# Performance work log

Measured on AMD Instinct MI355X. Metric: run time of the kernel, lower is better.

The kernel has to match this reference:

```python
import jax, jax.numpy as jnp
import numpy as np

D_IN = 1024
D_OUT = 1024
N = 4096


def setup_inputs() -> dict:
    key = jax.random.key(0)
    kx, kq, kk, kv = jax.random.split(key, 4)
    s = 1.0 / np.sqrt(D_IN)
    return {
        "x": jax.random.normal(kx, (N, D_IN), dtype=jnp.float32),
        # nn.Linear weights stored as [d_out, d_in]
        "wq": jax.random.uniform(kq, (D_OUT, D_IN), dtype=jnp.float32, minval=-s, maxval=s),
        "wk": jax.random.uniform(kk, (D_OUT, D_IN), dtype=jnp.float32, minval=-s, maxval=s),
        "wv": jax.random.uniform(kv, (D_OUT, D_IN), dtype=jnp.float32, minval=-s, maxval=s),
    }


def reference(x, wq, wk, wv):
    q = x @ wq.T  # [N, d_out]
    k = x @ wk.T
    v = x @ wv.T
    scores = q @ k.T  # [N, N]
    weights = jax.nn.softmax(scores / jnp.sqrt(jnp.asarray(k.shape[-1], x.dtype)), axis=-1)
    return weights @ v  # [N, d_out]
```

## Files before the change

kernel.cpp:

```cpp
#include <hip/hip_runtime.h>
#include <cstdint>

#define NTOK 4096
#define DMODEL 1024

typedef __bf16 bf16x8 __attribute__((ext_vector_type(8)));
typedef float f32x4 __attribute__((ext_vector_type(4)));

__device__ __forceinline__ unsigned short f32_to_bf16(float f) {
    unsigned int u = __float_as_uint(f);
    unsigned int r = 0x7FFFu + ((u >> 16) & 1u);
    return (unsigned short)((u + r) >> 16);
}

__global__ __launch_bounds__(256) void cvt_f32_bf16(const float* __restrict__ in,
                                                    unsigned short* __restrict__ out,
                                                    int n4) {
    int i = blockIdx.x * 256 + threadIdx.x;
    if (i >= n4) return;
    float4 v = reinterpret_cast<const float4*>(in)[i];
    ushort4 o;
    o.x = f32_to_bf16(v.x);
    o.y = f32_to_bf16(v.y);
    o.z = f32_to_bf16(v.z);
    o.w = f32_to_bf16(v.w);
    reinterpret_cast<ushort4*>(out)[i] = o;
}

#define BM 128
#define BN 128
#define BK 64

#define EPI_F32 0
#define EPI_BF16 1
#define EPI_BF16T 2

template <int EPI>
__global__ __launch_bounds__(256, 2) void gemm_nt(
    const unsigned short* __restrict__ A, const unsigned short* __restrict__ B,
    void* __restrict__ C, int K, int lda, int ldb, int ldc) {
    __shared__ __align__(16) unsigned short As[BM * BK];
    __shared__ __align__(16) unsigned short Bs[BN * BK];

    const int tid = threadIdx.x;
    const int lane = tid & 63;
    const int wave = tid >> 6;
    const int wr = wave >> 1, wc = wave & 1;

    const unsigned short* Ablk = A + (size_t)blockIdx.y * BM * lda;
    const unsigned short* Bblk = B + (size_t)blockIdx.x * BN * ldb;

    f32x4 acc[4][4] = {};

    for (int k0 = 0; k0 < K; k0 += BK) {
#pragma unroll
        for (int i = 0; i < 4; ++i) {
            const int c = tid + i * 256;
            const int row = c >> 3;
            const int jl = (c & 7) ^ (row & 7);
            const unsigned short* ga = Ablk + (size_t)row * lda + (k0 + jl * 8);
            const unsigned short* gb = Bblk + (size_t)row * ldb + (k0 + jl * 8);
            __builtin_amdgcn_global_load_lds(
                (const __attribute__((address_space(1))) void*)ga,
                (__attribute__((address_space(3))) void*)(&As[c * 8]), 16, 0, 0);
            __builtin_amdgcn_global_load_lds(
                (const __attribute__((address_space(1))) void*)gb,
                (__attribute__((address_space(3))) void*)(&Bs[c * 8]), 16, 0, 0);
        }
        __syncthreads();

#pragma unroll
        for (int ks = 0; ks < 2; ++ks) {
            bf16x8 af[4], bfr[4];
#pragma unroll
            for (int m = 0; m < 4; ++m) {
                const int row = wr * 64 + m * 16 + (lane & 15);
                const int ch = (ks * 4 + (lane >> 4)) ^ (row & 7);
                af[m] = *reinterpret_cast<const bf16x8*>(
                    reinterpret_cast<const char*>(As) + row * 128 + ch * 16);
            }
#pragma unroll
            for (int n = 0; n < 4; ++n) {
                const int row = wc * 64 + n * 16 + (lane & 15);
                const int ch = (ks * 4 + (lane >> 4)) ^ (row & 7);
                bfr[n] = *reinterpret_cast<const bf16x8*>(
                    reinterpret_cast<const char*>(Bs) + row * 128 + ch * 16);
            }
#pragma unroll
            for (int m = 0; m < 4; ++m)
#pragma unroll
                for (int n = 0; n < 4; ++n)
                    acc[m][n] = __builtin_amdgcn_mfma_f32_16x16x32_bf16(
                        af[m], bfr[n], acc[m][n], 0, 0, 0);
        }
        __syncthreads();
    }

    const int col0 = blockIdx.x * BN + wc * 64 + (lane & 15);
    const int row0 = blockIdx.y * BM + wr * 64 + ((lane >> 4) << 2);

    if (EPI == EPI_F32) {
        float* Cf = reinterpret_cast<float*>(C);
#pragma unroll
        for (int m = 0; m < 4; ++m)
#pragma unroll
            for (int n = 0; n < 4; ++n)
#pragma unroll
                for (int r = 0; r < 4; ++r)
                    Cf[(size_t)(row0 + m * 16 + r) * ldc + (col0 + n * 16)] = acc[m][n][r];
    } else if (EPI == EPI_BF16) {
        unsigned short* Cb = reinterpret_cast<unsigned short*>(C);
#pragma unroll
        for (int m = 0; m < 4; ++m)
#pragma unroll
            for (int n = 0; n < 4; ++n)
#pragma unroll
                for (int r = 0; r < 4; ++r)
                    Cb[(size_t)(row0 + m * 16 + r) * ldc + (col0 + n * 16)] =
                        f32_to_bf16(acc[m][n][r]);
    } else {
        unsigned short* Cb = reinterpret_cast<unsigned short*>(C);
#pragma unroll
        for (int m = 0; m < 4; ++m)
#pragma unroll
            for (int n = 0; n < 4; ++n) {
                ushort4 o;
                o.x = f32_to_bf16(acc[m][n][0]);
                o.y = f32_to_bf16(acc[m][n][1]);
                o.z = f32_to_bf16(acc[m][n][2]);
                o.w = f32_to_bf16(acc[m][n][3]);
                *reinterpret_cast<ushort4*>(
                    &Cb[(size_t)(col0 + n * 16) * ldc + (row0 + m * 16)]) = o;
            }
    }
}

__global__ __launch_bounds__(256) void softmax_rows(float* __restrict__ S, int N) {
    const int row = blockIdx.x;
    float* s = S + (size_t)row * N;
    const int t = threadIdx.x;

    float v[16];
    float mx = -1e30f;
#pragma unroll
    for (int i = 0; i < 4; ++i) {
        float4 x = reinterpret_cast<const float4*>(s)[t + i * 256];
        v[i * 4 + 0] = x.x;
        v[i * 4 + 1] = x.y;
        v[i * 4 + 2] = x.z;
        v[i * 4 + 3] = x.w;
        mx = fmaxf(mx, fmaxf(fmaxf(x.x, x.y), fmaxf(x.z, x.w)));
    }
#pragma unroll
    for (int off = 32; off; off >>= 1) mx = fmaxf(mx, __shfl_xor(mx, off));
    __shared__ float redm[4];
    if (!(t & 63)) redm[t >> 6] = mx;
    __syncthreads();
    mx = fmaxf(fmaxf(redm[0], redm[1]), fmaxf(redm[2], redm[3]));

    float sum = 0.f;
#pragma unroll
    for (int i = 0; i < 16; ++i) {
        v[i] = __expf((v[i] - mx) * 0.03125f);
        sum += v[i];
    }
#pragma unroll
    for (int off = 32; off; off >>= 1) sum += __shfl_xor(sum, off);
    __shared__ float reds[4];
    if (!(t & 63)) reds[t >> 6] = sum;
    __syncthreads();
    sum = (reds[0] + reds[1]) + (reds[2] + reds[3]);
    const float inv = 1.0f / sum;

    unsigned short* p = reinterpret_cast<unsigned short*>(s);
#pragma unroll
    for (int i = 0; i < 4; ++i) {
        ushort4 o;
        o.x = f32_to_bf16(v[i * 4 + 0] * inv);
        o.y = f32_to_bf16(v[i * 4 + 1] * inv);
        o.z = f32_to_bf16(v[i * 4 + 2] * inv);
        o.w = f32_to_bf16(v[i * 4 + 3] * inv);
        reinterpret_cast<ushort4*>(p)[t + i * 256] = o;
    }
}

extern "C" void kernel_launch(void* const* d_in, const int* in_sizes, int n_in,
                              void* d_out, int out_size, void* d_ws, size_t ws_size,
                              hipStream_t stream) {
    (void)in_sizes; (void)n_in; (void)out_size; (void)ws_size;
    const float* x = (const float*)d_in[0];
    const float* wq = (const float*)d_in[1];
    const float* wk = (const float*)d_in[2];
    const float* wv = (const float*)d_in[3];
    float* out = (float*)d_out;

    const size_t MB = 1ull << 20;
    char* w = (char*)d_ws;
    unsigned short* xb  = (unsigned short*)(w + 0 * MB);
    unsigned short* wqb = (unsigned short*)(w + 8 * MB);
    unsigned short* wkb = (unsigned short*)(w + 10 * MB);
    unsigned short* wvb = (unsigned short*)(w + 12 * MB);
    unsigned short* Qb  = (unsigned short*)(w + 14 * MB);
    unsigned short* Kb  = (unsigned short*)(w + 22 * MB);
    unsigned short* Vt  = (unsigned short*)(w + 30 * MB);
    float* S            = (float*)(w + 38 * MB);

    cvt_f32_bf16<<<4096, 256, 0, stream>>>(x, xb, (NTOK * DMODEL) / 4);
    cvt_f32_bf16<<<1024, 256, 0, stream>>>(wq, wqb, (DMODEL * DMODEL) / 4);
    cvt_f32_bf16<<<1024, 256, 0, stream>>>(wk, wkb, (DMODEL * DMODEL) / 4);
    cvt_f32_bf16<<<1024, 256, 0, stream>>>(wv, wvb, (DMODEL * DMODEL) / 4);

    dim3 gqkv(DMODEL / BN, NTOK / BM);
    gemm_nt<EPI_BF16><<<gqkv, 256, 0, stream>>>(xb, wqb, Qb, DMODEL, DMODEL, DMODEL, DMODEL);
    gemm_nt<EPI_BF16><<<gqkv, 256, 0, stream>>>(xb, wkb, Kb, DMODEL, DMODEL, DMODEL, DMODEL);
    gemm_nt<EPI_BF16T><<<gqkv, 256, 0, stream>>>(xb, wvb, Vt, DMODEL, DMODEL, DMODEL, NTOK);

    dim3 gs(NTOK / BN, NTOK / BM);
    gemm_nt<EPI_F32><<<gs, 256, 0, stream>>>(Qb, Kb, S, DMODEL, DMODEL, DMODEL, NTOK);

    softmax_rows<<<NTOK, 256, 0, stream>>>(S, NTOK);

    dim3 gpv(DMODEL / BN, NTOK / BM);
    gemm_nt<EPI_F32><<<gpv, 256, 0, stream>>>((const unsigned short*)S, Vt, out,
                                              NTOK, 2 * NTOK, NTOK, DMODEL);
}
```

Baseline: 264.0 us.

## Fuse QKV projections into one GEMM and split-K the PV GEMM with atomics

Concatenates the three bf16 weight matrices so Q, K and V come from a single 24x32-block GEMM launch, with Q and K interleaved in one [N,2048] buffer and V written transposed. The PV GEMM, which had only 256 blocks, is split four ways along K with fp32 atomic adds into an output that is zeroed first. This cuts launch count and raises parallelism on the small-grid GEMMs, at the cost of an extra memset, atomic traffic and a nondeterministic summation order.

```diff
diff --git a/kernel.cpp b/kernel.cpp
--- a/kernel.cpp
+++ b/kernel.cpp
@@ -31,17 +31,47 @@
 #define BN 128
 #define BK 64
 
-#define EPI_F32 0
-#define EPI_BF16 1
-#define EPI_BF16T 2
-
-template <int EPI>
-__global__ __launch_bounds__(256, 2) void gemm_nt(
+#define STAGE_TILES(Ablk, lda, Bblk, ldb, k0)                                        \
+    _Pragma("unroll") for (int i = 0; i < 4; ++i) {                                  \
+        const int c = tid + i * 256;                                                 \
+        const int row = c >> 3;                                                      \
+        const int jl = (c & 7) ^ (row & 7);                                          \
+        const unsigned short* ga = (Ablk) + (size_t)row * (lda) + ((k0) + jl * 8);   \
+        const unsigned short* gb = (Bblk) + (size_t)row * (ldb) + ((k0) + jl * 8);   \
+        __builtin_amdgcn_global_load_lds(                                            \
+            (const __attribute__((address_space(1))) void*)ga,                       \
+            (__attribute__((address_space(3))) void*)(&As[c * 8]), 16, 0, 0);        \
+        __builtin_amdgcn_global_load_lds(                                            \
+            (const __attribute__((address_space(1))) void*)gb,                       \
+            (__attribute__((address_space(3))) void*)(&Bs[c * 8]), 16, 0, 0);        \
+    }
+
+#define COMPUTE_TILE()                                                               \
+    _Pragma("unroll") for (int ks = 0; ks < 2; ++ks) {                               \
+        bf16x8 af[4], bfr[4];                                                        \
+        _Pragma("unroll") for (int m = 0; m < 4; ++m) {                              \
+            const int row = wr * 64 + m * 16 + (lane & 15);                          \
+            const int ch = (ks * 4 + (lane >> 4)) ^ (row & 7);                       \
+            af[m] = *reinterpret_cast<const bf16x8*>(                                \
+                reinterpret_cast<const char*>(As) + row * 128 + ch * 16);            \
+        }                                                                            \
+        _Pragma("unroll") for (int n = 0; n < 4; ++n) {                              \
+            const int row = wc * 64 + n * 16 + (lane & 15);                          \
+            const int ch = (ks * 4 + (lane >> 4)) ^ (row & 7);                       \
+            bfr[n] = *reinterpret_cast<const bf16x8*>(                               \
+                reinterpret_cast<const char*>(Bs) + row * 128 + ch * 16);            \
+        }                                                                            \
+        _Pragma("unroll") for (int m = 0; m < 4; ++m)                                \
+            _Pragma("unroll") for (int n = 0; n < 4; ++n)                            \
+                acc[m][n] = __builtin_amdgcn_mfma_f32_16x16x32_bf16(                 \
+                    af[m], bfr[n], acc[m][n], 0, 0, 0);                              \
+    }
+
+__global__ __launch_bounds__(256, 2) void gemm_nt_f32(
     const unsigned short* __restrict__ A, const unsigned short* __restrict__ B,
-    void* __restrict__ C, int K, int lda, int ldb, int ldc) {
+    float* __restrict__ C, int K, int lda, int ldb, int ldc) {
     __shared__ __align__(16) unsigned short As[BM * BK];
     __shared__ __align__(16) unsigned short Bs[BN * BK];
-
     const int tid = threadIdx.x;
     const int lane = tid & 63;
     const int wave = tid >> 6;
@@ -49,77 +79,62 @@
 
     const unsigned short* Ablk = A + (size_t)blockIdx.y * BM * lda;
     const unsigned short* Bblk = B + (size_t)blockIdx.x * BN * ldb;
-
     f32x4 acc[4][4] = {};
 
     for (int k0 = 0; k0 < K; k0 += BK) {
-#pragma unroll
-        for (int i = 0; i < 4; ++i) {
-            const int c = tid + i * 256;
-            const int row = c >> 3;
-            const int jl = (c & 7) ^ (row & 7);
-            const unsigned short* ga = Ablk + (size_t)row * lda + (k0 + jl * 8);
-            const unsigned short* gb = Bblk + (size_t)row * ldb + (k0 + jl * 8);
-            __builtin_amdgcn_global_load_lds(
-                (const __attribute__((address_space(1))) void*)ga,
-                (__attribute__((address_space(3))) void*)(&As[c * 8]), 16, 0, 0);
-            __builtin_amdgcn_global_load_lds(
-                (const __attribute__((address_space(1))) void*)gb,
-                (__attribute__((address_space(3))) void*)(&Bs[c * 8]), 16, 0, 0);
-        }
-        __syncthreads();
-
-#pragma unroll
-        for (int ks = 0; ks < 2; ++ks) {
-            bf16x8 af[4], bfr[4];
-#pragma unroll
-            for (int m = 0; m < 4; ++m) {
-                const int row = wr * 64 + m * 16 + (lane & 15);
-                const int ch = (ks * 4 + (lane >> 4)) ^ (row & 7);
-                af[m] = *reinterpret_cast<const bf16x8*>(
-                    reinterpret_cast<const char*>(As) + row * 128 + ch * 16);
-            }
-#pragma unroll
-            for (int n = 0; n < 4; ++n) {
-                const int row = wc * 64 + n * 16 + (lane & 15);
-                const int ch = (ks * 4 + (lane >> 4)) ^ (row & 7);
-                bfr[n] = *reinterpret_cast<const bf16x8*>(
-                    reinterpret_cast<const char*>(Bs) + row * 128 + ch * 16);
-            }
-#pragma unroll
-            for (int m = 0; m < 4; ++m)
-#pragma unroll
-                for (int n = 0; n < 4; ++n)
-                    acc[m][n] = __builtin_amdgcn_mfma_f32_16x16x32_bf16(
-                        af[m], bfr[n], acc[m][n], 0, 0, 0);
-        }
+        STAGE_TILES(Ablk, lda, Bblk, ldb, k0)
+        __syncthreads();
+        COMPUTE_TILE()
         __syncthreads();
     }
 
     const int col0 = blockIdx.x * BN + wc * 64 + (lane & 15);
     const int row0 = blockIdx.y * BM + wr * 64 + ((lane >> 4) << 2);
-
-    if (EPI == EPI_F32) {
-        float* Cf = reinterpret_cast<float*>(C);
+#pragma unroll
+    for (int m = 0; m < 4; ++m)
+#pragma unroll
+        for (int n = 0; n < 4; ++n)
+#pragma unroll
+            for (int r = 0; r < 4; ++r)
+                C[(size_t)(row0 + m * 16 + r) * ldc + (col0 + n * 16)] = acc[m][n][r];
+}
+
+__global__ __launch_bounds__(256, 2) void gemm_qkv(
+    const unsigned short* __restrict__ xb, const unsigned short* __restrict__ Wb,
+    unsigned short* __restrict__ QK, unsigned short* __restrict__ Vt) {
+    __shared__ __align__(16) unsigned short As[BM * BK];
+    __shared__ __align__(16) unsigned short Bs[BN * BK];
+    const int tid = threadIdx.x;
+    const int lane = tid & 63;
+    const int wave = tid >> 6;
+    const int wr = wave >> 1, wc = wave & 1;
+    const int bx = blockIdx.x;
+
+    const unsigned short* Ablk = xb + (size_t)blockIdx.y * BM * DMODEL;
+    const unsigned short* Bblk = Wb + (size_t)bx * BN * DMODEL;
+    f32x4 acc[4][4] = {};
+
+    for (int k0 = 0; k0 < DMODEL; k0 += BK) {
+        STAGE_TILES(Ablk, DMODEL, Bblk, DMODEL, k0)
+        __syncthreads();
+        COMPUTE_TILE()
+        __syncthreads();
+    }
+
+    const int colw = wc * 64 + (lane & 15);
+    const int row0 = blockIdx.y * BM + wr * 64 + ((lane >> 4) << 2);
+    if (bx < 16) {
+        const int col0 = bx * 128 + colw;
 #pragma unroll
         for (int m = 0; m < 4; ++m)
 #pragma unroll
             for (int n = 0; n < 4; ++n)
 #pragma unroll
                 for (int r = 0; r < 4; ++r)
-                    Cf[(size_t)(row0 + m * 16 + r) * ldc + (col0 + n * 16)] = acc[m][n][r];
-    } else if (EPI == EPI_BF16) {
-        unsigned short* Cb = reinterpret_cast<unsigned short*>(C);
-#pragma unroll
-        for (int m = 0; m < 4; ++m)
-#pragma unroll
-            for (int n = 0; n < 4; ++n)
-#pragma unroll
-                for (int r = 0; r < 4; ++r)
-                    Cb[(size_t)(row0 + m * 16 + r) * ldc + (col0 + n * 16)] =
+                    QK[(size_t)(row0 + m * 16 + r) * 2048 + (col0 + n * 16)] =
                         f32_to_bf16(acc[m][n][r]);
     } else {
-        unsigned short* Cb = reinterpret_cast<unsigned short*>(C);
+        const int vrow0 = (bx - 16) * 128 + colw;
 #pragma unroll
         for (int m = 0; m < 4; ++m)
 #pragma unroll
@@ -130,9 +145,44 @@
                 o.z = f32_to_bf16(acc[m][n][2]);
                 o.w = f32_to_bf16(acc[m][n][3]);
                 *reinterpret_cast<ushort4*>(
-                    &Cb[(size_t)(col0 + n * 16) * ldc + (row0 + m * 16)]) = o;
+                    &Vt[(size_t)(vrow0 + n * 16) * NTOK + (row0 + m * 16)]) = o;
             }
     }
+}
+
+__global__ __launch_bounds__(256, 2) void gemm_pv_splitk(
+    const unsigned short* __restrict__ P, const unsigned short* __restrict__ Vt,
+    float* __restrict__ C) {
+    __shared__ __align__(16) unsigned short As[BM * BK];
+    __shared__ __align__(16) unsigned short Bs[BN * BK];
+    const int tid = threadIdx.x;
+    const int lane = tid & 63;
+    const int wave = tid >> 6;
+    const int wr = wave >> 1, wc = wave & 1;
+
+    const unsigned short* Ablk = P + (size_t)blockIdx.y * BM * (2 * NTOK);
+    const unsigned short* Bblk = Vt + (size_t)blockIdx.x * BN * NTOK;
+    f32x4 acc[4][4] = {};
+
+    const int kbeg = blockIdx.z * (NTOK / 4);
+    const int kend = kbeg + NTOK / 4;
+    for (int k0 = kbeg; k0 < kend; k0 += BK) {
+        STAGE_TILES(Ablk, 2 * NTOK, Bblk, NTOK, k0)
+        __syncthreads();
+        COMPUTE_TILE()
+        __syncthreads();
+    }
+
+    const int col0 = blockIdx.x * BN + wc * 64 + (lane & 15);
+    const int row0 = blockIdx.y * BM + wr * 64 + ((lane >> 4) << 2);
+#pragma unroll
+    for (int m = 0; m < 4; ++m)
+#pragma unroll
+        for (int n = 0; n < 4; ++n)
+#pragma unroll
+            for (int r = 0; r < 4; ++r)
+                unsafeAtomicAdd(&C[(size_t)(row0 + m * 16 + r) * DMODEL + (col0 + n * 16)],
+                                acc[m][n][r]);
 }
 
 __global__ __launch_bounds__(256) void softmax_rows(float* __restrict__ S, int N) {
@@ -196,31 +246,23 @@
 
     const size_t MB = 1ull << 20;
     char* w = (char*)d_ws;
-    unsigned short* xb  = (unsigned short*)(w + 0 * MB);
-    unsigned short* wqb = (unsigned short*)(w + 8 * MB);
-    unsigned short* wkb = (unsigned short*)(w + 10 * MB);
-    unsigned short* wvb = (unsigned short*)(w + 12 * MB);
-    unsigned short* Qb  = (unsigned short*)(w + 14 * MB);
-    unsigned short* Kb  = (unsigned short*)(w + 22 * MB);
-    unsigned short* Vt  = (unsigned short*)(w + 30 * MB);
-    float* S            = (float*)(w + 38 * MB);
+    unsigned short* xb = (unsigned short*)(w + 0 * MB);
+    unsigned short* Wb = (unsigned short*)(w + 8 * MB);
+    unsigned short* QK = (unsigned short*)(w + 14 * MB);
+    unsigned short* Vt = (unsigned short*)(w + 30 * MB);
+    float* S           = (float*)(w + 38 * MB);
 
     cvt_f32_bf16<<<4096, 256, 0, stream>>>(x, xb, (NTOK * DMODEL) / 4);
-    cvt_f32_bf16<<<1024, 256, 0, stream>>>(wq, wqb, (DMODEL * DMODEL) / 4);
-    cvt_f32_bf16<<<1024, 256, 0, stream>>>(wk, wkb, (DMODEL * DMODEL) / 4);
-    cvt_f32_bf16<<<1024, 256, 0, stream>>>(wv, wvb, (DMODEL * DMODEL) / 4);
-
-    dim3 gqkv(DMODEL / BN, NTOK / BM);
-    gemm_nt<EPI_BF16><<<gqkv, 256, 0, stream>>>(xb, wqb, Qb, DMODEL, DMODEL, DMODEL, DMODEL);
-    gemm_nt<EPI_BF16><<<gqkv, 256, 0, stream>>>(xb, wkb, Kb, DMODEL, DMODEL, DMODEL, DMODEL);
-    gemm_nt<EPI_BF16T><<<gqkv, 256, 0, stream>>>(xb, wvb, Vt, DMODEL, DMODEL, DMODEL, NTOK);
-
-    dim3 gs(NTOK / BN, NTOK / BM);
-    gemm_nt<EPI_F32><<<gs, 256, 0, stream>>>(Qb, Kb, S, DMODEL, DMODEL, DMODEL, NTOK);
+    cvt_f32_bf16<<<1024, 256, 0, stream>>>(wq, Wb, (DMODEL * DMODEL) / 4);
+    cvt_f32_bf16<<<1024, 256, 0, stream>>>(wk, Wb + DMODEL * DMODEL, (DMODEL * DMODEL) / 4);
+    cvt_f32_bf16<<<1024, 256, 0, stream>>>(wv, Wb + 2 * DMODEL * DMODEL, (DMODEL * DMODEL) / 4);
+
+    gemm_qkv<<<dim3(24, 32), 256, 0, stream>>>(xb, Wb, QK, Vt);
+
+    gemm_nt_f32<<<dim3(32, 32), 256, 0, stream>>>(QK, QK + 1024, S, DMODEL, 2048, 2048, NTOK);
 
     softmax_rows<<<NTOK, 256, 0, stream>>>(S, NTOK);
 
-    dim3 gpv(DMODEL / BN, NTOK / BM);
-    gemm_nt<EPI_F32><<<gpv, 256, 0, stream>>>((const unsigned short*)S, Vt, out,
-                                              NTOK, 2 * NTOK, NTOK, DMODEL);
-}
+    hipMemsetAsync(d_out, 0, (size_t)NTOK * DMODEL * sizeof(float), stream);
+    gemm_pv_splitk<<<dim3(8, 32, 4), 256, 0, stream>>>((const unsigned short*)S, Vt, out);
+}
```

Measured after the change: 251.4 us. 1.05x faster.
